# Optimization experiments

Measured on AMD Instinct MI355X. Metric: run time of the kernel, lower is better.

## Reference

```python
import jax, jax.numpy as jnp
import numpy as np

N, S, E = 8, 1024, 768
H = 12
D = E // H  # head_dim = 64
FF = 4 * E
EPS = 1e-5


def setup_inputs() -> dict:
    key = jax.random.key(0)
    ks = jax.random.split(key, 12)
    s = lambda fan_in: 1.0 / np.sqrt(fan_in)
    return {
        "x": jax.random.normal(ks[0], (N, S, E), dtype=jnp.float32),
        "ln1_g": jnp.ones((E,), jnp.float32),
        "ln1_b": jnp.zeros((E,), jnp.float32),
        "ln2_g": jnp.ones((E,), jnp.float32),
        "ln2_b": jnp.zeros((E,), jnp.float32),
        "w_attn": jax.random.normal(ks[1], (E, 3 * E), jnp.float32) * s(E),
        "b_attn": jax.random.normal(ks[2], (3 * E,), jnp.float32) * 0.02,
        "w_proj": jax.random.normal(ks[3], (E, E), jnp.float32) * s(E),
        "b_proj": jax.random.normal(ks[4], (E,), jnp.float32) * 0.02,
        "w_fc": jax.random.normal(ks[5], (E, FF), jnp.float32) * s(E),
        "b_fc": jax.random.normal(ks[6], (FF,), jnp.float32) * 0.02,
        "w_fc2": jax.random.normal(ks[7], (FF, E), jnp.float32) * s(FF),
        "b_fc2": jax.random.normal(ks[8], (E,), jnp.float32) * 0.02,
    }


def _layernorm(x, g, b):
    mu = jnp.mean(x, axis=-1, keepdims=True)
    var = jnp.var(x, axis=-1, keepdims=True)
    return (x - mu) * jax.lax.rsqrt(var + EPS) * g + b


def reference(x, ln1_g, ln1_b, ln2_g, ln2_b, w_attn, b_attn, w_proj, b_proj,
              w_fc, b_fc, w_fc2, b_fc2):
    # --- attention branch (pre-LN) ---
    h = _layernorm(x, ln1_g, ln1_b)
    qkv = h @ w_attn + b_attn                       # [N,S,3E]
    q, k, v = jnp.split(qkv, 3, axis=-1)
    q = q.reshape(N, S, H, D).transpose(0, 2, 1, 3)  # [N,H,S,D]
    k = k.reshape(N, S, H, D).transpose(0, 2, 1, 3)
    v = v.reshape(N, S, H, D).transpose(0, 2, 1, 3)
    attn = jnp.einsum('nhsd,nhtd->nhst', q, k) * (1.0 / np.sqrt(D))
    causal = jnp.tril(jnp.ones((S, S), bool))
    attn = jnp.where(causal, attn, -jnp.inf)
    p = jax.nn.softmax(attn, axis=-1)
    out = jnp.einsum('nhst,nhtd->nhsd', p, v)        # [N,H,S,D]
    out = out.transpose(0, 2, 1, 3).reshape(N, S, E)
    x = x + (out @ w_proj + b_proj)
    # --- MLP branch ---
    h2 = _layernorm(x, ln2_g, ln2_b)
    ff = jax.nn.gelu(h2 @ w_fc + b_fc, approximate=False)  # exact GELU (torch nn.GELU default)
    x = x + (ff @ w_fc2 + b_fc2)
    return x
```

## Files before the change

### kernel.cpp

```cpp
#include <hip/hip_runtime.h>
#include <hip/hip_bf16.h>
#include <stdint.h>

#define S_LEN 1024
#define E_DIM 768
#define H_N   12
#define FF_DIM 3072

typedef __hip_bfloat16 bf16;
using short8  = __attribute__((ext_vector_type(8))) short;
using short4v = __attribute__((ext_vector_type(4))) short;
using f32x4   = __attribute__((ext_vector_type(4))) float;

__device__ __forceinline__ void async_cp16(const void* g, void* l) {
  __builtin_amdgcn_global_load_lds(
      (__attribute__((address_space(1))) void*)(g),
      (__attribute__((address_space(3))) void*)(l), 16, 0, 0);
}

__global__ __launch_bounds__(256) void wcastT_all(
    const float* __restrict__ wa, const float* __restrict__ wp,
    const float* __restrict__ wf, const float* __restrict__ wf2,
    bf16* __restrict__ oa, bf16* __restrict__ op,
    bf16* __restrict__ of, bf16* __restrict__ of2) {
  __shared__ float t[32][33];
  int bid = blockIdx.x;
  const float* w; bf16* wt; int K, N, bx, by;
  if (bid < 1728)      { w = wa;  wt = oa;  K = 768;  N = 2304; int r = bid;        bx = r % 72; by = r / 72; }
  else if (bid < 2304) { w = wp;  wt = op;  K = 768;  N = 768;  int r = bid - 1728; bx = r % 24; by = r / 24; }
  else if (bid < 4608) { w = wf;  wt = of;  K = 768;  N = 3072; int r = bid - 2304; bx = r % 96; by = r / 96; }
  else                 { w = wf2; wt = of2; K = 3072; N = 768;  int r = bid - 4608; bx = r % 24; by = r / 24; }
  int x = threadIdx.x & 31;
  int y = threadIdx.x >> 5;
  for (int i = y; i < 32; i += 8)
    t[i][x] = w[(size_t)(by * 32 + i) * N + bx * 32 + x];
  __syncthreads();
  for (int i = y; i < 32; i += 8)
    wt[(size_t)(bx * 32 + i) * K + by * 32 + x] = __float2bfloat16(t[x][i]);
}

__global__ __launch_bounds__(256) void ln_rows(const float* __restrict__ x,
                                               const float* __restrict__ g,
                                               const float* __restrict__ b,
                                               bf16* __restrict__ out) {
  int row = blockIdx.x;
  int tid = threadIdx.x;
  const float* xr = x + (size_t)row * E_DIM;
  float v0 = xr[tid], v1 = xr[tid + 256], v2 = xr[tid + 512];
  float s = v0 + v1 + v2;
  float ss = v0 * v0 + v1 * v1 + v2 * v2;
  for (int o = 32; o > 0; o >>= 1) {
    s  += __shfl_down(s, o);
    ss += __shfl_down(ss, o);
  }
  __shared__ float ps[4], pq[4];
  int wv = tid >> 6;
  if ((tid & 63) == 0) { ps[wv] = s; pq[wv] = ss; }
  __syncthreads();
  s  = ps[0] + ps[1] + ps[2] + ps[3];
  ss = pq[0] + pq[1] + pq[2] + pq[3];
  float mu  = s * (1.0f / E_DIM);
  float var = ss * (1.0f / E_DIM) - mu * mu;
  float rs  = rsqrtf(var + 1e-5f);
  bf16* orow = out + (size_t)row * E_DIM;
  orow[tid]       = __float2bfloat16((v0 - mu) * rs * g[tid]       + b[tid]);
  orow[tid + 256] = __float2bfloat16((v1 - mu) * rs * g[tid + 256] + b[tid + 256]);
  orow[tid + 512] = __float2bfloat16((v2 - mu) * rs * g[tid + 512] + b[tid + 512]);
}

__global__ __launch_bounds__(256) void scatter_v(const bf16* __restrict__ qkv,
                                                 bf16* __restrict__ vtb) {
  int blk = blockIdx.x;
  int n = blk >> 7, soct = blk & 127;
  int tid = threadIdx.x;
  for (int j = tid; j < 768; j += 256) {
    int h = j >> 6, d = j & 63;
    const bf16* src = qkv + ((size_t)(n * 1024 + soct * 8)) * 2304 + 1536 + h * 64 + d;
    short8 v;
#pragma unroll
    for (int i = 0; i < 8; i++)
      v[i] = __builtin_bit_cast(short, src[(size_t)i * 2304]);
    *(short8*)&vtb[((((size_t)n * 12 + h) * 128 + soct) * 64 + d) * 8] = v;
  }
}

template <int MODE>
__global__ __launch_bounds__(512, 2) void gemm8(
    const bf16* __restrict__ A, const bf16* __restrict__ Bt,
    const float* __restrict__ bias, bf16* __restrict__ outb,
    int M, int N, int K) {
  __shared__ bf16 lA[2][16384];
  __shared__ bf16 lB[2][16384];
  int tid = threadIdx.x;
  int w = tid >> 6, lane = tid & 63;
  int quad = lane >> 4, l16 = lane & 15;
  int wr = w >> 2, wc = w & 3;
  int gx = N >> 8;
  int flat = blockIdx.x;
  int y8 = flat & 7;
  int q2 = flat >> 3;
  int bx = q2 % gx;
  int by = (q2 / gx) * 8 + y8;
  int m0 = by << 8, n0 = bx << 8;

  f32x4 acc[8][4];
#pragma unroll
  for (int i = 0; i < 8; i++)
#pragma unroll
    for (int j = 0; j < 4; j++)
#pragma unroll
      for (int r = 0; r < 4; r++) acc[i][j][r] = 0.f;

  int xs = l16 & 7;
  int ko0 = (quad ^ xs) << 3;
  int ko1 = ((4 + quad) ^ xs) << 3;
  int sgo = ((tid & 7) ^ ((tid >> 3) & 7)) << 3;
  size_t aRB = (size_t)(m0 + (tid >> 3)) * K + sgo;
  size_t bRB = (size_t)(n0 + ((tid >> 8) << 6) + ((tid >> 3) & 31)) * K + sgo;
  int aD = tid * 8;
  int bD = ((tid >> 8) << 12) + (tid & 255) * 8;

  auto stA = [&](int buf, int mh, int kt) {
#pragma unroll
    for (int p = 0; p < 2; ++p)
      async_cp16(A + aRB + (size_t)(mh * 64 + p * 128) * K + (size_t)kt * 64,
                 &lA[buf][aD + mh * 4096 + p * 8192]);
  };
  auto stB = [&](int buf, int nh, int kt) {
#pragma unroll
    for (int p = 0; p < 2; ++p)
      async_cp16(Bt + bRB + (size_t)(nh * 32 + p * 128) * K + (size_t)kt * 64,
                 &lB[buf][bD + nh * 2048 + p * 8192]);
  };

  short8 af[4][2], b0f[2][2], b1f[2][2];

#define LD_A(BUF, MH)                                                      \
  {                                                                        \
    _Pragma("unroll") for (int i = 0; i < 4; ++i) {                        \
      const bf16* bp = &lA[BUF][(wr * 128 + (MH)*64 + i * 16 + l16) * 64]; \
      af[i][0] = *(const short8*)&bp[ko0];                                 \
      af[i][1] = *(const short8*)&bp[ko1];                                 \
    }                                                                      \
  }
#define LD_B(BUF, NH, DST)                                                 \
  {                                                                        \
    _Pragma("unroll") for (int j = 0; j < 2; ++j) {                        \
      const bf16* bp = &lB[BUF][(wc * 64 + (NH)*32 + j * 16 + l16) * 64];  \
      DST[j][0] = *(const short8*)&bp[ko0];                                \
      DST[j][1] = *(const short8*)&bp[ko1];                                \
    }                                                                      \
  }
#define DO_MFMA(MH, NH, BSRC)                                              \
  {                                                                        \
    __builtin_amdgcn_s_setprio(1);                                         \
    _Pragma("unroll") for (int ks = 0; ks < 2; ++ks)                       \
        _Pragma("unroll") for (int i = 0; i < 4; ++i)                      \
            _Pragma("unroll") for (int j = 0; j < 2; ++j)                  \
                acc[(MH)*4 + i][(NH)*2 + j] =                              \
        __builtin_amdgcn_mfma_f32_16x16x32_bf16(                           \
            BSRC[j][ks], af[i][ks], acc[(MH)*4 + i][(NH)*2 + j], 0, 0, 0); \
    __builtin_amdgcn_s_setprio(0);                                         \
  }
#define BAR() __builtin_amdgcn_s_barrier()
#define LGKM0() asm volatile("s_waitcnt lgkmcnt(0)" ::: "memory")
#define VM6() asm volatile("s_waitcnt vmcnt(6)" ::: "memory")
#define VM0() asm volatile("s_waitcnt vmcnt(0)" ::: "memory")

  stA(0, 0, 0); stA(0, 1, 0); stB(0, 0, 0); stB(0, 1, 0);
  stA(1, 0, 1); stB(1, 1, 1); stA(1, 1, 1);
  VM6();
  BAR();

  int nit = K >> 7;
  for (int it = 0; it < nit; ++it) {
    int kt1 = 2 * it + 1, ktA = 2 * it + 2, ktB = 2 * it + 3;
    bool more = (it + 1 < nit);
    LD_A(0, 0); LD_B(0, 0, b0f);
    stB(1, 0, kt1);
    BAR(); LGKM0(); DO_MFMA(0, 0, b0f); BAR();
    LD_B(0, 1, b1f);
    if (more) stA(0, 0, ktA);
    BAR(); LGKM0(); DO_MFMA(0, 1, b1f); BAR();
    LD_A(0, 1);
    if (more) stB(0, 1, ktA);
    BAR(); LGKM0(); DO_MFMA(1, 1, b1f); BAR();
    LD_B(0, 0, b0f);
    if (more) { stA(0, 1, ktA); VM6(); } else { VM0(); }
    BAR(); LGKM0(); DO_MFMA(1, 0, b0f); BAR();
    LD_A(1, 0); LD_B(1, 0, b0f);
    if (more) stB(0, 0, ktA);
    BAR(); LGKM0(); DO_MFMA(0, 0, b0f); BAR();
    LD_B(1, 1, b1f);
    if (more) stA(1, 0, ktB);
    BAR(); LGKM0(); DO_MFMA(0, 1, b1f); BAR();
    LD_A(1, 1);
    if (more) stB(1, 1, ktB);
    BAR(); LGKM0(); DO_MFMA(1, 1, b1f); BAR();
    LD_B(1, 0, b0f);
    if (more) { stA(1, 1, ktB); VM6(); }
    BAR(); LGKM0(); DO_MFMA(1, 0, b0f); BAR();
  }

#pragma unroll
  for (int nj = 0; nj < 4; ++nj) {
    int colb = n0 + wc * 64 + nj * 16 + quad * 4;
    f32x4 b4 = *(const f32x4*)&bias[colb];
    float sc = (MODE == 1 && colb < 768) ? 0.125f : 1.0f;
#pragma unroll
    for (int mi = 0; mi < 8; ++mi) {
      int row = m0 + wr * 128 + mi * 16 + l16;
      f32x4 v = acc[mi][nj] + b4;
      short4v pk;
      if (MODE == 1) {
        for (int r = 0; r < 4; r++)
          pk[r] = __builtin_bit_cast(short, __float2bfloat16(v[r] * sc));
      } else {
        for (int r = 0; r < 4; r++) {
          float x = v[r];
          float t = x * (1.59576912161f + 0.0713548162726f * x * x);
          float g = x * __builtin_amdgcn_rcpf(1.0f + __expf(-t));
          pk[r] = __builtin_bit_cast(short, __float2bfloat16(g));
        }
      }
      *(short4v*)&outb[(size_t)row * N + colb] = pk;
    }
  }
#undef LD_A
#undef LD_B
#undef DO_MFMA
#undef BAR
#undef LGKM0
#undef VM6
#undef VM0
}

__global__ __launch_bounds__(256) void gemm_bt64(
    const bf16* __restrict__ A, const bf16* __restrict__ Bt,
    const float* __restrict__ bias, const float* __restrict__ resid,
    float* __restrict__ outf, int M, int N, int K) {
  __shared__ bf16 As[2][128 * 64];
  __shared__ bf16 Bs[2][64 * 64];
  int tid = threadIdx.x;
  int wave = tid >> 6, lane = tid & 63;
  int quad = lane >> 4, l16 = lane & 15;
  int gx = N >> 6;
  int flat = blockIdx.x;
  int y8 = flat & 7;
  int q2 = flat >> 3;
  int bx = q2 % gx;
  int by = (q2 / gx) * 8 + y8;
  int m0 = by * 128, n0 = bx * 64;
  int wm = wave * 32;
  f32x4 acc[2][4];
  for (int i = 0; i < 2; i++)
    for (int j = 0; j < 4; j++)
      for (int r = 0; r < 4; r++) acc[i][j][r] = 0.f;

  int xs = l16 & 7;
  int srow = tid >> 3;
  int scg = (((tid & 7) ^ (srow & 7)) << 3);
  const bf16* aptr = A  + (size_t)(m0 + srow) * K + scg;
  const bf16* bptr = Bt + (size_t)(n0 + srow) * K + scg;
  int ldst = tid * 8;

#pragma unroll
  for (int t = 0; t < 4; t++)
    async_cp16(aptr + (size_t)t * 32 * K, &As[0][ldst + t * 2048]);
#pragma unroll
  for (int t = 0; t < 2; t++)
    async_cp16(bptr + (size_t)t * 32 * K, &Bs[0][ldst + t * 2048]);

  int nkb = K >> 6;
  for (int ik = 0; ik < nkb; ++ik) {
    int cur = ik & 1;
    if (ik + 1 < nkb) {
      size_t ko = (size_t)(ik + 1) * 64;
#pragma unroll
      for (int t = 0; t < 4; t++)
        async_cp16(aptr + ko + (size_t)t * 32 * K, &As[cur ^ 1][ldst + t * 2048]);
#pragma unroll
      for (int t = 0; t < 2; t++)
        async_cp16(bptr + ko + (size_t)t * 32 * K, &Bs[cur ^ 1][ldst + t * 2048]);
      asm volatile("s_waitcnt vmcnt(6)" ::: "memory");
    } else {
      asm volatile("s_waitcnt vmcnt(0)" ::: "memory");
    }
    __builtin_amdgcn_s_barrier();
    asm volatile("" ::: "memory");
#pragma unroll
    for (int ks = 0; ks < 2; ks++) {
      int ko2 = (((ks * 4 + quad) ^ xs) << 3);
      short8 af[2], bfr[4];
      for (int i = 0; i < 2; i++)
        af[i] = *(const short8*)&As[cur][(wm + i * 16 + l16) * 64 + ko2];
      for (int j = 0; j < 4; j++)
        bfr[j] = *(const short8*)&Bs[cur][(j * 16 + l16) * 64 + ko2];
      for (int i = 0; i < 2; i++)
        for (int j = 0; j < 4; j++)
          acc[i][j] = __builtin_amdgcn_mfma_f32_16x16x32_bf16(
              bfr[j], af[i], acc[i][j], 0, 0, 0);
    }
    asm volatile("" ::: "memory");
    __builtin_amdgcn_s_barrier();
  }

  for (int j = 0; j < 4; j++) {
    int colb = n0 + j * 16 + quad * 4;
    f32x4 b4 = *(const f32x4*)&bias[colb];
    for (int i = 0; i < 2; i++) {
      int row = m0 + wm + i * 16 + l16;
      size_t idx = (size_t)row * N + colb;
      f32x4 rv = *(const f32x4*)&resid[idx];
      *(f32x4*)&outf[idx] = acc[i][j] + b4 + rv;
    }
  }
}

__global__ __launch_bounds__(256) void attn_fwd(
    const bf16* __restrict__ qkv, const bf16* __restrict__ vg,
    bf16* __restrict__ out) {
  __shared__ bf16 kt2[2][8 * 64 * 8];
  __shared__ bf16 vt2[2][8 * 64 * 8];
  __shared__ bf16 pba[4][16 * 68];
  __shared__ bf16 pbb[4][16 * 68];
  int flat = blockIdx.x;
  int xcd = flat & 7;
  int j = flat >> 3;
  int a = j & 7;
  int g = j >> 3;
  int nh = xcd * 12 + g;
  int b = 15 - a;
  int n = nh / H_N, h = nh % H_N;
  int tid = threadIdx.x, wave = tid >> 6, lane = tid & 63;
  int quad = lane >> 4, l16 = lane & 15;
  const bf16* qp = qkv + (size_t)n * S_LEN * 2304 + (size_t)h * 64;
  const bf16* vp = vg + (size_t)nh * 128 * 64 * 8;
  int qra = a * 64 + wave * 16;
  int qrb = b * 64 + wave * 16;

  short8 qfa[2], qfb[2];
  qfa[0] = *(const short8*)&qp[(size_t)(qra + l16) * 2304 + quad * 8];
  qfa[1] = *(const short8*)&qp[(size_t)(qra + l16) * 2304 + 32 + quad * 8];
  qfb[0] = *(const short8*)&qp[(size_t)(qrb + l16) * 2304 + quad * 8];
  qfb[1] = *(const short8*)&qp[(size_t)(qrb + l16) * 2304 + 32 + quad * 8];

  const bf16* kbase = qkv + ((size_t)n * S_LEN + (tid & 63)) * 2304 + 768 +
                      h * 64 + ((tid >> 6) << 3);
  const bf16* vbase = vp + (((size_t)(tid >> 6) * 64) + (tid & 63)) * 8;

  f32x4 oaa[4], oab[4];
  for (int dt = 0; dt < 4; dt++)
    for (int r = 0; r < 4; r++) { oaa[dt][r] = 0.f; oab[dt][r] = 0.f; }
  float lia = 0.f, lib = 0.f;

  {
    bf16* lk = &kt2[0][0] + tid * 8;
    bf16* lv = &vt2[0][0] + tid * 8;
#pragma unroll
    for (int t = 0; t < 2; ++t) {
      async_cp16(kbase + t * 32, lk + t * 2048);
      async_cp16(vbase + (size_t)t * 2048, lv + t * 2048);
    }
  }

  for (int kb = 0; kb <= b; ++kb) {
    bool act_a = (kb <= a);
    int cur = kb & 1;
    __syncthreads();

    short8 kf[2][4], vf[2][4];
#pragma unroll
    for (int ks = 0; ks < 2; ks++)
      for (int nt = 0; nt < 4; nt++) {
        kf[ks][nt] = *(const short8*)
            &kt2[cur][(size_t)((ks * 4 + quad) * 64 + nt * 16 + l16) * 8];
        vf[ks][nt] = *(const short8*)
            &vt2[cur][(size_t)((ks * 4 + quad) * 64 + nt * 16 + l16) * 8];
      }
    if (kb < b) {
      bf16* lk = &kt2[cur ^ 1][0] + tid * 8;
      bf16* lv = &vt2[cur ^ 1][0] + tid * 8;
      size_t kko = (size_t)(kb + 1) * 64 * 2304;
      size_t vko = (size_t)(kb + 1) * 4096;
#pragma unroll
      for (int t = 0; t < 2; ++t) {
        async_cp16(kbase + kko + t * 32, lk + t * 2048);
        async_cp16(vbase + vko + (size_t)t * 2048, lv + t * 2048);
      }
    }

    f32x4 sb4[4], sa4[4];
    for (int nt = 0; nt < 4; nt++) {
      for (int r = 0; r < 4; r++) { sb4[nt][r] = -10.f; sa4[nt][r] = -10.f; }
      for (int ks = 0; ks < 2; ks++) {
        sb4[nt] = __builtin_amdgcn_mfma_f32_16x16x32_bf16(kf[ks][nt], qfb[ks],
                                                          sb4[nt], 0, 0, 0);
        if (act_a)
          sa4[nt] = __builtin_amdgcn_mfma_f32_16x16x32_bf16(kf[ks][nt], qfa[ks],
                                                            sa4[nt], 0, 0, 0);
      }
    }
    if (kb == b) {
      int ql = wave * 16 + l16;
      for (int nt = 0; nt < 4; nt++)
        for (int r = 0; r < 4; r++)
          if (nt * 16 + quad * 4 + r > ql) sb4[nt][r] = -INFINITY;
    }
    if (kb == a) {
      int ql = wave * 16 + l16;
      for (int nt = 0; nt < 4; nt++)
        for (int r = 0; r < 4; r++)
          if (nt * 16 + quad * 4 + r > ql) sa4[nt][r] = -INFINITY;
    }

    float rsb = 0.f;
    for (int nt = 0; nt < 4; nt++)
      for (int r = 0; r < 4; r++) {
        float p = __expf(sb4[nt][r]);
        sb4[nt][r] = p;
        rsb += p;
      }
    rsb += __shfl_xor(rsb, 16);
    rsb += __shfl_xor(rsb, 32);
    lib += rsb;
    bf16* pwb = pbb[wave];
    for (int nt = 0; nt < 4; nt++) {
      short4v pk;
      for (int r = 0; r < 4; r++)
        pk[r] = __builtin_bit_cast(short, __float2bfloat16(sb4[nt][r]));
      *(short4v*)&pwb[l16 * 68 + nt * 16 + quad * 4] = pk;
    }
    if (act_a) {
      float rsa = 0.f;
      for (int nt = 0; nt < 4; nt++)
        for (int r = 0; r < 4; r++) {
          float p = __expf(sa4[nt][r]);
          sa4[nt][r] = p;
          rsa += p;
        }
      rsa += __shfl_xor(rsa, 16);
      rsa += __shfl_xor(rsa, 32);
      lia += rsa;
      bf16* pwa = pba[wave];
      for (int nt = 0; nt < 4; nt++) {
        short4v pk;
        for (int r = 0; r < 4; r++)
          pk[r] = __builtin_bit_cast(short, __float2bfloat16(sa4[nt][r]));
        *(short4v*)&pwa[l16 * 68 + nt * 16 + quad * 4] = pk;
      }
    }
    asm volatile("s_waitcnt lgkmcnt(0)" ::: "memory");

    for (int ks = 0; ks < 2; ks++) {
      short8 pfb = *(const short8*)&pbb[wave][l16 * 68 + ks * 32 + quad * 8];
      short8 pfa;
      if (act_a) pfa = *(const short8*)&pba[wave][l16 * 68 + ks * 32 + quad * 8];
      for (int dt = 0; dt < 4; dt++) {
        oab[dt] = __builtin_amdgcn_mfma_f32_16x16x32_bf16(vf[ks][dt], pfb,
                                                          oab[dt], 0, 0, 0);
        if (act_a)
          oaa[dt] = __builtin_amdgcn_mfma_f32_16x16x32_bf16(vf[ks][dt], pfa,
                                                            oaa[dt], 0, 0, 0);
      }
    }
  }

  float inva = 1.0f / lia, invb = 1.0f / lib;
  int ta = n * S_LEN + qra + l16;
  int tb = n * S_LEN + qrb + l16;
  for (int dt = 0; dt < 4; dt++) {
    short4v ova, ovb;
    for (int r = 0; r < 4; r++) {
      ova[r] = __builtin_bit_cast(short, __float2bfloat16(oaa[dt][r] * inva));
      ovb[r] = __builtin_bit_cast(short, __float2bfloat16(oab[dt][r] * invb));
    }
    *(short4v*)&out[(size_t)ta * E_DIM + h * 64 + dt * 16 + quad * 4] = ova;
    *(short4v*)&out[(size_t)tb * E_DIM + h * 64 + dt * 16 + quad * 4] = ovb;
  }
}

extern "C" void kernel_launch(void* const* d_in, const int* in_sizes, int n_in,
                              void* d_out, int out_size, void* d_ws, size_t ws_size,
                              hipStream_t stream) {
  (void)in_sizes; (void)n_in; (void)out_size; (void)ws_size;
  const float* x      = (const float*)d_in[0];
  const float* ln1_g  = (const float*)d_in[1];
  const float* ln1_b  = (const float*)d_in[2];
  const float* ln2_g  = (const float*)d_in[3];
  const float* ln2_b  = (const float*)d_in[4];
  const float* w_attn = (const float*)d_in[5];
  const float* b_attn = (const float*)d_in[6];
  const float* w_proj = (const float*)d_in[7];
  const float* b_proj = (const float*)d_in[8];
  const float* w_fc   = (const float*)d_in[9];
  const float* b_fc   = (const float*)d_in[10];
  const float* w_fc2  = (const float*)d_in[11];
  const float* b_fc2  = (const float*)d_in[12];
  float* out = (float*)d_out;

  char* ws = (char*)d_ws;
  bf16* wt_attn = (bf16*)(ws);
  bf16* wt_proj = (bf16*)(ws + 3538944);
  bf16* wt_fc   = (bf16*)(ws + 4718592);
  bf16* wt_fc2  = (bf16*)(ws + 9437184);
  bf16* hbuf    = (bf16*)(ws + 14155776);
  float* x2     = (float*)(ws + 26738688);
  bf16* qkvb    = (bf16*)(ws + 51904512);
  bf16* vtb     = (bf16*)(ws + 89653248);
  bf16* ao      = hbuf;
  bf16* ff      = qkvb;

  dim3 blk(256);
  wcastT_all<<<dim3(6912), blk, 0, stream>>>(w_attn, w_proj, w_fc, w_fc2,
                                             wt_attn, wt_proj, wt_fc, wt_fc2);

  ln_rows<<<8192, blk, 0, stream>>>(x, ln1_g, ln1_b, hbuf);

  gemm8<1><<<dim3(288), dim3(512), 0, stream>>>(
      hbuf, wt_attn, b_attn, qkvb, 8192, 2304, 768);

  scatter_v<<<dim3(1024), blk, 0, stream>>>(qkvb, vtb);

  attn_fwd<<<dim3(768), blk, 0, stream>>>(qkvb, vtb, ao);

  gemm_bt64<<<dim3(12 * 64), blk, 0, stream>>>(
      ao, wt_proj, b_proj, x, x2, 8192, 768, 768);

  ln_rows<<<8192, blk, 0, stream>>>(x2, ln2_g, ln2_b, hbuf);

  gemm8<2><<<dim3(384), dim3(512), 0, stream>>>(
      hbuf, wt_fc, b_fc, ff, 8192, 3072, 768);

  gemm_bt64<<<dim3(12 * 64), blk, 0, stream>>>(
      ff, wt_fc2, b_fc2, x2, out, 8192, 768, 3072);
}
```

Measured before the change: 378.7 us.

## Shrink gemm8 tile to 256x128 and rework its async load pipeline

The 8-wave GEMM used for the QKV and FC1 projections now computes 256x128 output tiles instead of 256x256. That halves the B shared-memory buffer and the accumulator registers and doubles the grid (576 and 768 blocks), which should fill the 256 CUs better than 288 and 384 blocks. The interleaved load/MFMA schedule is rewritten into four phases per iteration with new wait counts. The cost is more A-tile refetch traffic and less data reuse per block.

Measured after the change: 360.6 us. -4.8%, faster.

```diff
diff --git a/kernel.cpp b/kernel.cpp
--- a/kernel.cpp
+++ b/kernel.cpp
@@ -90,24 +90,24 @@
     const float* __restrict__ bias, bf16* __restrict__ outb,
     int M, int N, int K) {
   __shared__ bf16 lA[2][16384];
-  __shared__ bf16 lB[2][16384];
+  __shared__ bf16 lB[2][8192];
   int tid = threadIdx.x;
   int w = tid >> 6, lane = tid & 63;
   int quad = lane >> 4, l16 = lane & 15;
   int wr = w >> 2, wc = w & 3;
-  int gx = N >> 8;
+  int gx = N >> 7;
   int flat = blockIdx.x;
   int y8 = flat & 7;
   int q2 = flat >> 3;
   int bx = q2 % gx;
   int by = (q2 / gx) * 8 + y8;
-  int m0 = by << 8, n0 = bx << 8;
-
-  f32x4 acc[8][4];
+  int m0 = by << 8, n0 = bx << 7;
+
+  f32x4 acc[8][2];
 #pragma unroll
   for (int i = 0; i < 8; i++)
 #pragma unroll
-    for (int j = 0; j < 4; j++)
+    for (int j = 0; j < 2; j++)
 #pragma unroll
       for (int r = 0; r < 4; r++) acc[i][j][r] = 0.f;
 
@@ -116,95 +116,85 @@
   int ko1 = ((4 + quad) ^ xs) << 3;
   int sgo = ((tid & 7) ^ ((tid >> 3) & 7)) << 3;
   size_t aRB = (size_t)(m0 + (tid >> 3)) * K + sgo;
-  size_t bRB = (size_t)(n0 + ((tid >> 8) << 6) + ((tid >> 3) & 31)) * K + sgo;
+  size_t bRB = (size_t)(n0 + (tid >> 3)) * K + sgo;
   int aD = tid * 8;
-  int bD = ((tid >> 8) << 12) + (tid & 255) * 8;
+  int bD = tid * 8;
 
   auto stA = [&](int buf, int mh, int kt) {
 #pragma unroll
     for (int p = 0; p < 2; ++p)
-      async_cp16(A + aRB + (size_t)(mh * 64 + p * 128) * K + (size_t)kt * 64,
+      async_cp16(A + aRB + (size_t)(p * 128 + mh * 64) * K + (size_t)kt * 64,
                  &lA[buf][aD + mh * 4096 + p * 8192]);
   };
-  auto stB = [&](int buf, int nh, int kt) {
+  auto stB = [&](int buf, int kt) {
 #pragma unroll
     for (int p = 0; p < 2; ++p)
-      async_cp16(Bt + bRB + (size_t)(nh * 32 + p * 128) * K + (size_t)kt * 64,
-                 &lB[buf][bD + nh * 2048 + p * 8192]);
+      async_cp16(Bt + bRB + (size_t)(p * 64) * K + (size_t)kt * 64,
+                 &lB[buf][bD + p * 4096]);
   };
 
-  short8 af[4][2], b0f[2][2], b1f[2][2];
-
-#define LD_A(BUF, MH)                                                      \
-  {                                                                        \
-    _Pragma("unroll") for (int i = 0; i < 4; ++i) {                        \
-      const bf16* bp = &lA[BUF][(wr * 128 + (MH)*64 + i * 16 + l16) * 64]; \
-      af[i][0] = *(const short8*)&bp[ko0];                                 \
-      af[i][1] = *(const short8*)&bp[ko1];                                 \
-    }                                                                      \
-  }
-#define LD_B(BUF, NH, DST)                                                 \
-  {                                                                        \
-    _Pragma("unroll") for (int j = 0; j < 2; ++j) {                        \
-      const bf16* bp = &lB[BUF][(wc * 64 + (NH)*32 + j * 16 + l16) * 64];  \
-      DST[j][0] = *(const short8*)&bp[ko0];                                \
-      DST[j][1] = *(const short8*)&bp[ko1];                                \
-    }                                                                      \
-  }
-#define DO_MFMA(MH, NH, BSRC)                                              \
-  {                                                                        \
-    __builtin_amdgcn_s_setprio(1);                                         \
-    _Pragma("unroll") for (int ks = 0; ks < 2; ++ks)                       \
-        _Pragma("unroll") for (int i = 0; i < 4; ++i)                      \
-            _Pragma("unroll") for (int j = 0; j < 2; ++j)                  \
-                acc[(MH)*4 + i][(NH)*2 + j] =                              \
-        __builtin_amdgcn_mfma_f32_16x16x32_bf16(                           \
-            BSRC[j][ks], af[i][ks], acc[(MH)*4 + i][(NH)*2 + j], 0, 0, 0); \
-    __builtin_amdgcn_s_setprio(0);                                         \
+  short8 af[4][2], bf[2][2];
+
+#define LD_A(BUF, MH)                                                        \
+  {                                                                          \
+    _Pragma("unroll") for (int i = 0; i < 4; ++i) {                          \
+      const bf16* bp =                                                       \
+          &lA[BUF][(MH)*4096 + wr * 8192 + (i * 16 + l16) * 64];             \
+      af[i][0] = *(const short8*)&bp[ko0];                                   \
+      af[i][1] = *(const short8*)&bp[ko1];                                   \
+    }                                                                        \
+  }
+#define LD_B(BUF)                                                            \
+  {                                                                          \
+    _Pragma("unroll") for (int j = 0; j < 2; ++j) {                          \
+      int rb = wc * 32 + j * 16 + l16;                                       \
+      const bf16* bp = &lB[BUF][((rb >> 6) << 12) + ((rb & 63) << 6)];       \
+      bf[j][0] = *(const short8*)&bp[ko0];                                   \
+      bf[j][1] = *(const short8*)&bp[ko1];                                   \
+    }                                                                        \
+  }
+#define DO_MFMA(MH)                                                          \
+  {                                                                          \
+    __builtin_amdgcn_s_setprio(1);                                           \
+    _Pragma("unroll") for (int ks = 0; ks < 2; ++ks)                         \
+        _Pragma("unroll") for (int i = 0; i < 4; ++i)                        \
+            _Pragma("unroll") for (int j = 0; j < 2; ++j)                    \
+                acc[(MH)*4 + i][j] =                                         \
+        __builtin_amdgcn_mfma_f32_16x16x32_bf16(                             \
+            bf[j][ks], af[i][ks], acc[(MH)*4 + i][j], 0, 0, 0);              \
+    __builtin_amdgcn_s_setprio(0);                                           \
   }
 #define BAR() __builtin_amdgcn_s_barrier()
 #define LGKM0() asm volatile("s_waitcnt lgkmcnt(0)" ::: "memory")
-#define VM6() asm volatile("s_waitcnt vmcnt(6)" ::: "memory")
+#define VM4() asm volatile("s_waitcnt vmcnt(4)" ::: "memory")
 #define VM0() asm volatile("s_waitcnt vmcnt(0)" ::: "memory")
 
-  stA(0, 0, 0); stA(0, 1, 0); stB(0, 0, 0); stB(0, 1, 0);
-  stA(1, 0, 1); stB(1, 1, 1); stA(1, 1, 1);
-  VM6();
+  stA(0, 0, 0); stA(0, 1, 0); stB(0, 0);
+  stA(1, 0, 1); stB(1, 1);
+  VM4();
   BAR();
 
   int nit = K >> 7;
   for (int it = 0; it < nit; ++it) {
-    int kt1 = 2 * it + 1, ktA = 2 * it + 2, ktB = 2 * it + 3;
+    int ktA = 2 * it + 2, ktB = 2 * it + 3;
     bool more = (it + 1 < nit);
-    LD_A(0, 0); LD_B(0, 0, b0f);
-    stB(1, 0, kt1);
-    BAR(); LGKM0(); DO_MFMA(0, 0, b0f); BAR();
-    LD_B(0, 1, b1f);
-    if (more) stA(0, 0, ktA);
-    BAR(); LGKM0(); DO_MFMA(0, 1, b1f); BAR();
+    LD_A(0, 0); LD_B(0);
+    stA(1, 1, 2 * it + 1);
+    BAR(); LGKM0(); DO_MFMA(0); BAR();
     LD_A(0, 1);
-    if (more) stB(0, 1, ktA);
-    BAR(); LGKM0(); DO_MFMA(1, 1, b1f); BAR();
-    LD_B(0, 0, b0f);
-    if (more) { stA(0, 1, ktA); VM6(); } else { VM0(); }
-    BAR(); LGKM0(); DO_MFMA(1, 0, b0f); BAR();
-    LD_A(1, 0); LD_B(1, 0, b0f);
-    if (more) stB(0, 0, ktA);
-    BAR(); LGKM0(); DO_MFMA(0, 0, b0f); BAR();
-    LD_B(1, 1, b1f);
-    if (more) stA(1, 0, ktB);
-    BAR(); LGKM0(); DO_MFMA(0, 1, b1f); BAR();
+    if (more) { stA(0, 0, ktA); stB(0, ktA); VM4(); } else { VM0(); }
+    BAR(); LGKM0(); DO_MFMA(1); BAR();
+    LD_A(1, 0); LD_B(1);
+    if (more) stA(0, 1, ktA);
+    BAR(); LGKM0(); DO_MFMA(0); BAR();
     LD_A(1, 1);
-    if (more) stB(1, 1, ktB);
-    BAR(); LGKM0(); DO_MFMA(1, 1, b1f); BAR();
-    LD_B(1, 0, b0f);
-    if (more) { stA(1, 1, ktB); VM6(); }
-    BAR(); LGKM0(); DO_MFMA(1, 0, b0f); BAR();
-  }
-
-#pragma unroll
-  for (int nj = 0; nj < 4; ++nj) {
-    int colb = n0 + wc * 64 + nj * 16 + quad * 4;
+    if (more) { stA(1, 0, ktB); stB(1, ktB); VM4(); }
+    BAR(); LGKM0(); DO_MFMA(1); BAR();
+  }
+
+#pragma unroll
+  for (int nj = 0; nj < 2; ++nj) {
+    int colb = n0 + wc * 32 + nj * 16 + quad * 4;
     f32x4 b4 = *(const f32x4*)&bias[colb];
     float sc = (MODE == 1 && colb < 768) ? 0.125f : 1.0f;
 #pragma unroll
@@ -231,7 +221,7 @@
 #undef DO_MFMA
 #undef BAR
 #undef LGKM0
-#undef VM6
+#undef VM4
 #undef VM0
 }
 
@@ -517,7 +507,7 @@
 
   ln_rows<<<8192, blk, 0, stream>>>(x, ln1_g, ln1_b, hbuf);
 
-  gemm8<1><<<dim3(288), dim3(512), 0, stream>>>(
+  gemm8<1><<<dim3(576), dim3(512), 0, stream>>>(
       hbuf, wt_attn, b_attn, qkvb, 8192, 2304, 768);
 
   scatter_v<<<dim3(1024), blk, 0, stream>>>(qkvb, vtb);
@@ -529,7 +519,7 @@
 
   ln_rows<<<8192, blk, 0, stream>>>(x2, ln2_g, ln2_b, hbuf);
 
-  gemm8<2><<<dim3(384), dim3(512), 0, stream>>>(
+  gemm8<2><<<dim3(768), dim3(512), 0, stream>>>(
       hbuf, wt_fc, b_fc, ff, 8192, 3072, 768);
 
   gemm_bt64<<<dim3(12 * 64), blk, 0, stream>>>(
```
